# Kernel optimization log

Measured on AMD Instinct MI355X. Metric: run time of the kernel, lower is better.

Reference implementation:

```python
import jax, jax.numpy as jnp
import numpy as np

WS = 7   # window size
SS = 3   # shift size


def _ln(x, g, b):
    m = x.mean(-1, keepdims=True)
    v = ((x - m) ** 2).mean(-1, keepdims=True)
    return (x - m) / jnp.sqrt(v + 1e-5) * g + b


def setup_inputs() -> dict:
    key = jax.random.key(0)
    ks = jax.random.split(key, 8)
    B, H, W, C, nh = 64, 56, 56, 96, 3
    N = WS * WS
    x = jax.random.normal(ks[0], (B, H * W, C), jnp.float32)

    # Swin SW-MSA attention mask: [nW, N, N], 0 where attention is allowed, -100 otherwise
    img = np.zeros((H, W), np.int32)
    cnt = 0
    for hs in (slice(0, H - WS), slice(H - WS, H - SS), slice(H - SS, None)):
        for wsl in (slice(0, W - WS), slice(W - WS, W - SS), slice(W - SS, None)):
            img[hs, wsl] = cnt
            cnt += 1
    win = img.reshape(H // WS, WS, W // WS, WS).transpose(0, 2, 1, 3).reshape(-1, N)
    am = np.where(win[:, None, :] != win[:, :, None], -100.0, 0.0).astype(np.float32)

    # relative position index: [N, N] in [0, (2*WS-1)^2)
    coords = np.stack(np.meshgrid(np.arange(WS), np.arange(WS), indexing='ij')).reshape(2, -1)
    rel = (coords[:, :, None] - coords[:, None, :]).transpose(1, 2, 0)
    rel[..., 0] += WS - 1
    rel[..., 1] += WS - 1
    rel[..., 0] *= 2 * WS - 1
    rel_index = jnp.asarray(rel.sum(-1), jnp.int32)

    p = lambda k, sh: jax.random.normal(k, sh, jnp.float32) * 0.02
    return dict(
        x=x,
        attn_mask=jnp.asarray(am),
        rel_index=rel_index,
        norm1_g=jnp.ones((C,), jnp.float32), norm1_b=jnp.zeros((C,), jnp.float32),
        qkv_w=p(ks[1], (3 * C, C)), qkv_b=jnp.zeros((3 * C,), jnp.float32),
        rel_bias_table=p(ks[2], ((2 * WS - 1) ** 2, nh)),
        proj_w=p(ks[3], (C, C)), proj_b=jnp.zeros((C,), jnp.float32),
        norm2_g=jnp.ones((C,), jnp.float32), norm2_b=jnp.zeros((C,), jnp.float32),
        fc1_w=p(ks[4], (4 * C, C)), fc1_b=jnp.zeros((4 * C,), jnp.float32),
        fc2_w=p(ks[5], (C, 4 * C)), fc2_b=jnp.zeros((C,), jnp.float32),
        H=56, W=56,
    )


def reference(x, attn_mask, rel_index, norm1_g, norm1_b, qkv_w, qkv_b,
              rel_bias_table, proj_w, proj_b, norm2_g, norm2_b,
              fc1_w, fc1_b, fc2_w, fc2_b, H, W):
    B, L, C = x.shape
    nh = rel_bias_table.shape[1]
    d = C // nh
    N = WS * WS
    shortcut = x

    xn = _ln(x, norm1_g, norm1_b).reshape(B, H, W, C)
    # cyclic shift (H%WS==0, W%WS==0 so no padding needed)
    xs = jnp.roll(xn, (-SS, -SS), axis=(1, 2))
    # window partition -> [B*nW, N, C]
    xw = xs.reshape(B, H // WS, WS, W // WS, WS, C).transpose(0, 1, 3, 2, 4, 5).reshape(-1, N, C)
    B_ = xw.shape[0]
    nW = attn_mask.shape[0]

    qkv = (xw @ qkv_w.T + qkv_b).reshape(B_, N, 3, nh, d).transpose(2, 0, 3, 1, 4)
    q, k, v = qkv[0] * (d ** -0.5), qkv[1], qkv[2]  # [B_, nh, N, d]
    attn = jnp.einsum('bhnd,bhmd->bhnm', q, k)
    bias = rel_bias_table[rel_index.reshape(-1)].reshape(N, N, nh).transpose(2, 0, 1)
    attn = attn + bias[None]
    attn = attn.reshape(B_ // nW, nW, nh, N, N) + attn_mask[None, :, None]
    attn = jax.nn.softmax(attn.reshape(B_, nh, N, N), axis=-1)
    out = jnp.einsum('bhnm,bhmd->bhnd', attn, v).transpose(0, 2, 1, 3).reshape(B_, N, C)
    out = out @ proj_w.T + proj_b

    # window reverse + reverse cyclic shift
    xr = out.reshape(B, H // WS, W // WS, WS, WS, C).transpose(0, 1, 3, 2, 4, 5).reshape(B, H, W, C)
    xr = jnp.roll(xr, (SS, SS), axis=(1, 2)).reshape(B, L, C)

    x = shortcut + xr
    h = _ln(x, norm2_g, norm2_b)
    h = jax.nn.gelu(h @ fc1_w.T + fc1_b, approximate=False) @ fc2_w.T + fc2_b
    return x + h
```

## Files before the change

kernel.cpp:

```cpp
#include <hip/hip_runtime.h>
#include <hip/hip_bf16.h>

typedef __attribute__((ext_vector_type(8))) short short8;
typedef __attribute__((ext_vector_type(4))) float f32x4;

constexpr int HW = 56;

constexpr int SR    = 104;
constexpr int SVT   = 200;
constexpr int OFF_X = 0;
constexpr int OFF_Q = 64 * SR;
constexpr int OFF_K = 2 * 64 * SR;
constexpr int OFF_V = 3 * 64 * SR;
constexpr int POOLN = OFF_V + 32 * SVT;

constexpr int WQKV  = 0;
constexpr int WPROJ = 27648;
constexpr int WFC1  = 36864;
constexpr int WFC2  = 73728;
constexpr int WTOT  = 110592;

__device__ __forceinline__ ushort bfc(float f) {
  union { __hip_bfloat16 h; ushort u; } v;
  v.h = __float2bfloat16(f);
  return v.u;
}
__device__ __forceinline__ uint pk2(float a, float b) {
  union { __hip_bfloat162 h2; uint u; } v;
  v.h2 = __float22bfloat162_rn(make_float2(a, b));
  return v.u;
}
__device__ __forceinline__ void st4(short* p, float a, float b, float c, float d) {
  uint2 u; u.x = pk2(a, b); u.y = pk2(c, d);
  *(uint2*)p = u;
}
__device__ __forceinline__ short8 ldw8(const float* p) {
  float4 a = *(const float4*)p;
  float4 b = *(const float4*)(p + 4);
  short8 r;
  r[0] = (short)bfc(a.x); r[1] = (short)bfc(a.y); r[2] = (short)bfc(a.z); r[3] = (short)bfc(a.w);
  r[4] = (short)bfc(b.x); r[5] = (short)bfc(b.y); r[6] = (short)bfc(b.z); r[7] = (short)bfc(b.w);
  return r;
}
template<bool PRE>
__device__ __forceinline__ short8 wfrag(const short* wsb, int ts, int lane, const float* fsrc) {
  if constexpr (PRE) return *(const short8*)&wsb[(ts << 9) + lane * 8];
  else               return ldw8(fsrc);
}
__device__ __forceinline__ float gelu(float v) {
  return v / (1.0f + __expf(-1.702f * v));
}
__device__ __forceinline__ void stage9(const short* g0, short* l0, int wv, int lane) {
  #pragma unroll
  for (int s4 = 0; s4 < 3; ++s4) {
    int s = wv + 4 * s4;
    if (s < 9)
      __builtin_amdgcn_global_load_lds((const unsigned int*)(g0 + (s << 9) + lane * 8),
                                       (unsigned int*)(l0 + (s << 9)), 16, 0, 0);
  }
}

__global__ __launch_bounds__(256) void cvt_weights(
    const float* __restrict__ qkv_w, const float* __restrict__ proj_w,
    const float* __restrict__ fc1_w, const float* __restrict__ fc2_w,
    short* __restrict__ ws)
{
  int idx = blockIdx.x * 256 + threadIdx.x;
  if (idx >= WTOT) return;
  int j = idx & 7, lane = (idx >> 3) & 63;
  int cl = lane & 15;
  int g  = 8 * (lane >> 4) + j;
  float v;
  if (idx < WPROJ) {
    int ts = idx >> 9; int tile = ts / 3, s = ts - 3 * tile;
    v = qkv_w[(size_t)(16 * tile + cl) * 96 + 32 * s + g];
  } else if (idx < WFC1) {
    int ts = (idx - WPROJ) >> 9; int tile = ts / 3, s = ts - 3 * tile;
    v = proj_w[(size_t)(16 * tile + cl) * 96 + 32 * s + g];
  } else if (idx < WFC2) {
    int ts = (idx - WFC1) >> 9; int T = ts / 3, s = ts - 3 * T;
    int cn = T / 6, nt = T - 6 * cn;
    v = fc1_w[(size_t)(96 * cn + 16 * nt + cl) * 96 + 32 * s + g];
  } else {
    int ts = (idx - WFC2) >> 9; int T = ts / 3, s = ts - 3 * T;
    int cn = T / 6, nt = T - 6 * cn;
    v = fc2_w[(size_t)(16 * nt + cl) * 384 + 96 * cn + 32 * s + g];
  }
  ws[idx] = (short)bfc(v);
}

template<bool PRE>
__global__ __launch_bounds__(256, 3) void swin_mfma_kernel(
    const float* __restrict__ x,
    const float* __restrict__ attn_mask,
    const int*   __restrict__ rel_index,
    const float* __restrict__ n1g, const float* __restrict__ n1b,
    const float* __restrict__ qkv_w, const float* __restrict__ qkv_b,
    const float* __restrict__ rel_tab,
    const float* __restrict__ proj_w, const float* __restrict__ proj_b,
    const float* __restrict__ n2g, const float* __restrict__ n2b,
    const float* __restrict__ fc1_w, const float* __restrict__ fc1_b,
    const float* __restrict__ fc2_w, const float* __restrict__ fc2_b,
    const short* __restrict__ wsw,
    float* __restrict__ out)
{
  __shared__ alignas(16) short pool[POOLN];
  short* bufA = (short*)&pool[OFF_K];
  short* bufB = (short*)&pool[OFF_K + 4608];

  const int tid  = threadIdx.x;
  const int wv   = tid >> 6;
  const int lane = tid & 63;
  const int ln   = lane & 15;
  const int gq   = lane >> 4;
  const int bw   = blockIdx.x;
  const int b    = bw >> 6, widx = bw & 63;
  const int wr   = widx >> 3, wc = widx & 7;

  const f32x4 zf = {0.f, 0.f, 0.f, 0.f};
  const int qq = 16 * wv + ln;

  auto gbase = [&](int n) -> size_t {
    int i = n / 7, j = n - 7 * i;
    int h = wr * 7 + i + 3; if (h >= HW) h -= HW;
    int w = wc * 7 + j + 3; if (w >= HW) w -= HW;
    return ((size_t)b * (HW * HW) + (size_t)h * HW + w) * 96;
  };
  const size_t obase = gbase(qq < 49 ? qq : 48);

  float xraw[6][4];
  {
    if (qq < 49) {
      const float* xr = x + obase;
      #pragma unroll
      for (int nt = 0; nt < 6; ++nt) {
        float4 v = *(const float4*)&xr[16 * nt + 4 * gq];
        xraw[nt][0] = v.x; xraw[nt][1] = v.y; xraw[nt][2] = v.z; xraw[nt][3] = v.w;
      }
    } else {
      #pragma unroll
      for (int nt = 0; nt < 6; ++nt)
        xraw[nt][0] = xraw[nt][1] = xraw[nt][2] = xraw[nt][3] = 0.f;
    }
    float s1 = 0.f, s2 = 0.f;
    #pragma unroll
    for (int nt = 0; nt < 6; ++nt)
      #pragma unroll
      for (int r = 0; r < 4; ++r) { s1 += xraw[nt][r]; s2 += xraw[nt][r] * xraw[nt][r]; }
    s1 += __shfl_xor(s1, 16, 64); s1 += __shfl_xor(s1, 32, 64);
    s2 += __shfl_xor(s2, 16, 64); s2 += __shfl_xor(s2, 32, 64);
    float mean = s1 * (1.f / 96.f);
    float inv  = rsqrtf(s2 * (1.f / 96.f) - mean * mean + 1e-5f);
    #pragma unroll
    for (int nt = 0; nt < 6; ++nt) {
      float4 g4 = *(const float4*)&n1g[16 * nt + 4 * gq];
      float4 b4 = *(const float4*)&n1b[16 * nt + 4 * gq];
      st4(&pool[OFF_X + qq * SR + 16 * nt + 4 * gq],
          (xraw[nt][0] - mean) * inv * g4.x + b4.x,
          (xraw[nt][1] - mean) * inv * g4.y + b4.y,
          (xraw[nt][2] - mean) * inv * g4.z + b4.z,
          (xraw[nt][3] - mean) * inv * g4.w + b4.w);
    }
  }
  __syncthreads();

  {
    short8 af[3][4];
    #pragma unroll
    for (int s = 0; s < 3; ++s)
      #pragma unroll
      for (int m = 0; m < 4; ++m)
        af[s][m] = *(const short8*)&pool[OFF_X + (16 * m + ln) * SR + 32 * s + 8 * gq];

    for (int t = wv; t < 18; t += 4) {
      short8 wf[3];
      #pragma unroll
      for (int s = 0; s < 3; ++s)
        wf[s] = wfrag<PRE>(wsw + WQKV, t * 3 + s, lane,
                           qkv_w + (size_t)(16 * t + ln) * 96 + 32 * s + 8 * gq);
      int which = t / 6;
      if (which == 2) {
        int d  = 16 * (t - 12) + ln;
        float bv = qkv_b[192 + d];
        int dd = d & 31, hh = d >> 5;
        #pragma unroll
        for (int m = 0; m < 4; ++m) {
          f32x4 acc = zf;
          #pragma unroll
          for (int s = 0; s < 3; ++s)
            acc = __builtin_amdgcn_mfma_f32_16x16x32_bf16(af[s][m], wf[s], acc, 0, 0, 0);
          st4(&pool[OFF_V + dd * SVT + hh * 64 + 16 * m + 4 * gq],
              acc[0] + bv, acc[1] + bv, acc[2] + bv, acc[3] + bv);
        }
      } else {
        float4 b4 = *(const float4*)&qkv_b[16 * t + 4 * gq];
        #pragma unroll
        for (int m = 0; m < 4; ++m) {
          f32x4 acc = zf;
          #pragma unroll
          for (int s = 0; s < 3; ++s)
            acc = __builtin_amdgcn_mfma_f32_16x16x32_bf16(wf[s], af[s][m], acc, 0, 0, 0);
          int tok = 16 * m + ln;
          float v0 = acc[0] + b4.x, v1 = acc[1] + b4.y, v2 = acc[2] + b4.z, v3 = acc[3] + b4.w;
          if (which == 0) {
            const float sc_ = 0.17677669529663687f;
            st4(&pool[OFF_Q + tok * SR + 16 * t + 4 * gq], v0 * sc_, v1 * sc_, v2 * sc_, v3 * sc_);
          } else {
            st4(&pool[OFF_K + tok * SR + 16 * (t - 6) + 4 * gq], v0, v1, v2, v3);
          }
        }
      }
    }
  }
  __syncthreads();

  int   relvv[4][4];
  float maskb[4][4];
  {
    int qc = qq < 49 ? qq : 48;
    #pragma unroll
    for (int nt = 0; nt < 4; ++nt)
      #pragma unroll
      for (int r = 0; r < 4; ++r) {
        int key = 16 * nt + 4 * gq + r;
        if (key < 49) {
          int qk = qc * 49 + key;
          relvv[nt][r] = rel_index[qk];
          maskb[nt][r] = attn_mask[(size_t)widx * 2401 + qk];
        } else {
          relvv[nt][r] = 0;
          maskb[nt][r] = -1e30f;
        }
      }
  }

  for (int h = 0; h < 3; ++h) {
    short8 bq = *(const short8*)&pool[OFF_Q + qq * SR + h * 32 + 8 * gq];
    f32x4 sc[4];
    #pragma unroll
    for (int nt = 0; nt < 4; ++nt) {
      f32x4 bia;
      #pragma unroll
      for (int r = 0; r < 4; ++r)
        bia[r] = rel_tab[relvv[nt][r] * 3 + h] + maskb[nt][r];
      short8 ak = *(const short8*)&pool[OFF_K + (16 * nt + ln) * SR + h * 32 + 8 * gq];
      sc[nt] = __builtin_amdgcn_mfma_f32_16x16x32_bf16(ak, bq, bia, 0, 0, 0);
    }
    float pv[4][4];
    float sum = 0.f;
    #pragma unroll
    for (int nt = 0; nt < 4; ++nt)
      #pragma unroll
      for (int r = 0; r < 4; ++r) { pv[nt][r] = __expf(sc[nt][r]); sum += pv[nt][r]; }
    sum += __shfl_xor(sum, 16, 64);
    sum += __shfl_xor(sum, 32, 64);
    float inv = 1.f / sum;
    #pragma unroll
    for (int nt = 0; nt < 4; ++nt)
      st4(&pool[OFF_X + qq * SR + 16 * nt + 4 * gq],
          pv[nt][0] * inv, pv[nt][1] * inv, pv[nt][2] * inv, pv[nt][3] * inv);

    short8 bp0 = *(const short8*)&pool[OFF_X + qq * SR + 8 * gq];
    short8 bp1 = *(const short8*)&pool[OFF_X + qq * SR + 32 + 8 * gq];
    #pragma unroll
    for (int dt = 0; dt < 2; ++dt) {
      short8 av0 = *(const short8*)&pool[OFF_V + (16 * dt + ln) * SVT + h * 64 + 8 * gq];
      short8 av1 = *(const short8*)&pool[OFF_V + (16 * dt + ln) * SVT + h * 64 + 32 + 8 * gq];
      f32x4 o = __builtin_amdgcn_mfma_f32_16x16x32_bf16(av0, bp0, zf, 0, 0, 0);
      o = __builtin_amdgcn_mfma_f32_16x16x32_bf16(av1, bp1, o, 0, 0, 0);
      st4(&pool[OFF_Q + qq * SR + h * 32 + 16 * dt + 4 * gq], o[0], o[1], o[2], o[3]);
    }
  }

  short8 ao[3];
  #pragma unroll
  for (int s = 0; s < 3; ++s)
    ao[s] = *(const short8*)&pool[OFF_Q + qq * SR + 32 * s + 8 * gq];
  __syncthreads();

  if constexpr (PRE) stage9(wsw + WPROJ, bufA, wv, lane);
  __syncthreads();

  if constexpr (PRE) stage9(wsw + WPROJ + 9 * 512, bufB, wv, lane);
  float y[6][4];
  #pragma unroll
  for (int nt = 0; nt < 3; ++nt) {
    f32x4 acc = zf;
    #pragma unroll
    for (int s = 0; s < 3; ++s) {
      short8 wfr = PRE ? *(const short8*)&bufA[(nt * 3 + s) * 512 + lane * 8]
                       : ldw8(proj_w + (size_t)(16 * nt + ln) * 96 + 32 * s + 8 * gq);
      acc = __builtin_amdgcn_mfma_f32_16x16x32_bf16(wfr, ao[s], acc, 0, 0, 0);
    }
    float4 pb = *(const float4*)&proj_b[16 * nt + 4 * gq];
    y[nt][0] = acc[0] + pb.x + xraw[nt][0];
    y[nt][1] = acc[1] + pb.y + xraw[nt][1];
    y[nt][2] = acc[2] + pb.z + xraw[nt][2];
    y[nt][3] = acc[3] + pb.w + xraw[nt][3];
  }
  __syncthreads();

  if constexpr (PRE) stage9(wsw + WFC1, bufA, wv, lane);
  #pragma unroll
  for (int nt = 3; nt < 6; ++nt) {
    f32x4 acc = zf;
    #pragma unroll
    for (int s = 0; s < 3; ++s) {
      short8 wfr = PRE ? *(const short8*)&bufB[((nt - 3) * 3 + s) * 512 + lane * 8]
                       : ldw8(proj_w + (size_t)(16 * nt + ln) * 96 + 32 * s + 8 * gq);
      acc = __builtin_amdgcn_mfma_f32_16x16x32_bf16(wfr, ao[s], acc, 0, 0, 0);
    }
    float4 pb = *(const float4*)&proj_b[16 * nt + 4 * gq];
    y[nt][0] = acc[0] + pb.x + xraw[nt][0];
    y[nt][1] = acc[1] + pb.y + xraw[nt][1];
    y[nt][2] = acc[2] + pb.z + xraw[nt][2];
    y[nt][3] = acc[3] + pb.w + xraw[nt][3];
  }
  {
    float s1 = 0.f, s2 = 0.f;
    #pragma unroll
    for (int nt = 0; nt < 6; ++nt)
      #pragma unroll
      for (int r = 0; r < 4; ++r) { s1 += y[nt][r]; s2 += y[nt][r] * y[nt][r]; }
    s1 += __shfl_xor(s1, 16, 64); s1 += __shfl_xor(s1, 32, 64);
    s2 += __shfl_xor(s2, 16, 64); s2 += __shfl_xor(s2, 32, 64);
    float mean = s1 * (1.f / 96.f);
    float inv  = rsqrtf(s2 * (1.f / 96.f) - mean * mean + 1e-5f);
    #pragma unroll
    for (int nt = 0; nt < 6; ++nt) {
      float4 g4 = *(const float4*)&n2g[16 * nt + 4 * gq];
      float4 b4 = *(const float4*)&n2b[16 * nt + 4 * gq];
      st4(&pool[OFF_Q + qq * SR + 16 * nt + 4 * gq],
          (y[nt][0] - mean) * inv * g4.x + b4.x,
          (y[nt][1] - mean) * inv * g4.y + b4.y,
          (y[nt][2] - mean) * inv * g4.z + b4.z,
          (y[nt][3] - mean) * inv * g4.w + b4.w);
    }
  }
  short8 ay[3];
  #pragma unroll
  for (int s = 0; s < 3; ++s)
    ay[s] = *(const short8*)&pool[OFF_Q + qq * SR + 32 * s + 8 * gq];
  __syncthreads();

  f32x4 accO[6] = {zf, zf, zf, zf, zf, zf};
  for (int cn = 0; cn < 4; ++cn) {
    if constexpr (PRE) stage9(wsw + WFC1 + (cn * 18 + 9) * 512, bufB, wv, lane);
    #pragma unroll
    for (int nt = 0; nt < 3; ++nt) {
      f32x4 acc = zf;
      #pragma unroll
      for (int s = 0; s < 3; ++s) {
        short8 wfr = PRE ? *(const short8*)&bufA[(nt * 3 + s) * 512 + lane * 8]
                         : ldw8(fc1_w + (size_t)(96 * cn + 16 * nt + ln) * 96 + 32 * s + 8 * gq);
        acc = __builtin_amdgcn_mfma_f32_16x16x32_bf16(wfr, ay[s], acc, 0, 0, 0);
      }
      float4 b1 = *(const float4*)&fc1_b[96 * cn + 16 * nt + 4 * gq];
      st4(&pool[OFF_X + qq * SR + 16 * nt + 4 * gq],
          gelu(acc[0] + b1.x), gelu(acc[1] + b1.y),
          gelu(acc[2] + b1.z), gelu(acc[3] + b1.w));
    }
    __syncthreads();
    if constexpr (PRE) stage9(wsw + WFC2 + (cn * 18) * 512, bufA, wv, lane);
    #pragma unroll
    for (int nt = 3; nt < 6; ++nt) {
      f32x4 acc = zf;
      #pragma unroll
      for (int s = 0; s < 3; ++s) {
        short8 wfr = PRE ? *(const short8*)&bufB[((nt - 3) * 3 + s) * 512 + lane * 8]
                         : ldw8(fc1_w + (size_t)(96 * cn + 16 * nt + ln) * 96 + 32 * s + 8 * gq);
        acc = __builtin_amdgcn_mfma_f32_16x16x32_bf16(wfr, ay[s], acc, 0, 0, 0);
      }
      float4 b1 = *(const float4*)&fc1_b[96 * cn + 16 * nt + 4 * gq];
      st4(&pool[OFF_X + qq * SR + 16 * nt + 4 * gq],
          gelu(acc[0] + b1.x), gelu(acc[1] + b1.y),
          gelu(acc[2] + b1.z), gelu(acc[3] + b1.w));
    }
    short8 ah[3];
    #pragma unroll
    for (int s = 0; s < 3; ++s)
      ah[s] = *(const short8*)&pool[OFF_X + qq * SR + 32 * s + 8 * gq];
    __syncthreads();
    if constexpr (PRE) stage9(wsw + WFC2 + (cn * 18 + 9) * 512, bufB, wv, lane);
    #pragma unroll
    for (int nt = 0; nt < 3; ++nt) {
      #pragma unroll
      for (int s = 0; s < 3; ++s) {
        short8 wfr = PRE ? *(const short8*)&bufA[(nt * 3 + s) * 512 + lane * 8]
                         : ldw8(fc2_w + (size_t)(16 * nt + ln) * 384 + 96 * cn + 32 * s + 8 * gq);
        accO[nt] = __builtin_amdgcn_mfma_f32_16x16x32_bf16(wfr, ah[s], accO[nt], 0, 0, 0);
      }
    }
    __syncthreads();
    if constexpr (PRE) { if (cn < 3) stage9(wsw + WFC1 + ((cn + 1) * 18) * 512, bufA, wv, lane); }
    #pragma unroll
    for (int nt = 3; nt < 6; ++nt) {
      #pragma unroll
      for (int s = 0; s < 3; ++s) {
        short8 wfr = PRE ? *(const short8*)&bufB[((nt - 3) * 3 + s) * 512 + lane * 8]
                         : ldw8(fc2_w + (size_t)(16 * nt + ln) * 384 + 96 * cn + 32 * s + 8 * gq);
        accO[nt] = __builtin_amdgcn_mfma_f32_16x16x32_bf16(wfr, ah[s], accO[nt], 0, 0, 0);
      }
    }
    __syncthreads();
  }

  if (qq < 49) {
    float* dst = out + obase;
    #pragma unroll
    for (int nt = 0; nt < 6; ++nt) {
      float4 fb = *(const float4*)&fc2_b[16 * nt + 4 * gq];
      float4 v;
      v.x = y[nt][0] + accO[nt][0] + fb.x;
      v.y = y[nt][1] + accO[nt][1] + fb.y;
      v.z = y[nt][2] + accO[nt][2] + fb.z;
      v.w = y[nt][3] + accO[nt][3] + fb.w;
      *(float4*)&dst[16 * nt + 4 * gq] = v;
    }
  }
}

extern "C" void kernel_launch(void* const* d_in, const int* in_sizes, int n_in,
                              void* d_out, int out_size, void* d_ws, size_t ws_size,
                              hipStream_t stream) {
  const float* x         = (const float*)d_in[0];
  const float* attn_mask = (const float*)d_in[1];
  const int*   rel_index = (const int*)  d_in[2];
  const float* n1g       = (const float*)d_in[3];
  const float* n1b       = (const float*)d_in[4];
  const float* qkv_w     = (const float*)d_in[5];
  const float* qkv_b     = (const float*)d_in[6];
  const float* rel_tab   = (const float*)d_in[7];
  const float* proj_w    = (const float*)d_in[8];
  const float* proj_b    = (const float*)d_in[9];
  const float* n2g       = (const float*)d_in[10];
  const float* n2b       = (const float*)d_in[11];
  const float* fc1_w     = (const float*)d_in[12];
  const float* fc1_b     = (const float*)d_in[13];
  const float* fc2_w     = (const float*)d_in[14];
  const float* fc2_b     = (const float*)d_in[15];
  float* out = (float*)d_out;

  const int B = in_sizes[0] / (HW * HW * 96);
  const bool pre = ws_size >= (size_t)WTOT * 2;

  if (pre) {
    short* ws = (short*)d_ws;
    cvt_weights<<<(WTOT + 255) / 256, 256, 0, stream>>>(qkv_w, proj_w, fc1_w, fc2_w, ws);
    swin_mfma_kernel<true><<<B * 64, 256, 0, stream>>>(
        x, attn_mask, rel_index, n1g, n1b, qkv_w, qkv_b, rel_tab, proj_w, proj_b,
        n2g, n2b, fc1_w, fc1_b, fc2_w, fc2_b, (const short*)ws, out);
  } else {
    swin_mfma_kernel<false><<<B * 64, 256, 0, stream>>>(
        x, attn_mask, rel_index, n1g, n1b, qkv_w, qkv_b, rel_tab, proj_w, proj_b,
        n2g, n2b, fc1_w, fc1_b, fc2_w, fc2_b, (const short*)nullptr, out);
  }
}
```

Measured before the change: 170.1 us.

## Precompute combined bias/mask table, fold q scale into weights, add setprio

A new prep kernel builds a per-window, per-head table of relative-position bias plus attention mask, padded to 64 keys. The main kernel then reads one float4 per tile instead of gathering rel_tab through indices and adding the mask. The q scaling is folded into the converted qkv weights and bias. The MFMA regions are wrapped in s_setprio, and the divides in GELU and softmax become rcp intrinsics. This costs an extra kernel launch and about 2.4 MB of workspace, and it depends on the workspace being large enough.

```diff
diff --git a/kernel.cpp b/kernel.cpp
--- a/kernel.cpp
+++ b/kernel.cpp
@@ -19,6 +19,9 @@
 constexpr int WFC1  = 36864;
 constexpr int WFC2  = 73728;
 constexpr int WTOT  = 110592;
+constexpr int BIASN = 64 * 3 * 49 * 64;
+constexpr size_t WS_M1 = (size_t)WTOT * 2;
+constexpr size_t WS_M2 = WS_M1 + (size_t)BIASN * 4;
 
 __device__ __forceinline__ ushort bfc(float f) {
   union { __hip_bfloat16 h; ushort u; } v;
@@ -48,7 +51,7 @@
   else               return ldw8(fsrc);
 }
 __device__ __forceinline__ float gelu(float v) {
-  return v / (1.0f + __expf(-1.702f * v));
+  return v * __builtin_amdgcn_rcpf(1.0f + __expf(-1.702f * v));
 }
 __device__ __forceinline__ void stage9(const short* g0, short* l0, int wv, int lane) {
   #pragma unroll
@@ -74,6 +77,7 @@
   if (idx < WPROJ) {
     int ts = idx >> 9; int tile = ts / 3, s = ts - 3 * tile;
     v = qkv_w[(size_t)(16 * tile + cl) * 96 + 32 * s + g];
+    if (tile < 6) v *= 0.17677669529663687f;
   } else if (idx < WFC1) {
     int ts = (idx - WPROJ) >> 9; int tile = ts / 3, s = ts - 3 * tile;
     v = proj_w[(size_t)(16 * tile + cl) * 96 + 32 * s + g];
@@ -89,7 +93,26 @@
   ws[idx] = (short)bfc(v);
 }
 
-template<bool PRE>
+__global__ __launch_bounds__(256) void prep_bias(
+    const float* __restrict__ attn_mask, const int* __restrict__ rel_index,
+    const float* __restrict__ rel_tab, float* __restrict__ bias3)
+{
+  int idx = blockIdx.x * 256 + threadIdx.x;
+  if (idx >= BIASN) return;
+  int k = idx & 63;
+  int t = idx >> 6;
+  int q = t % 49;
+  int wh = t / 49;
+  int h = wh % 3, w = wh / 3;
+  float v = -1e30f;
+  if (k < 49) {
+    int qk = q * 49 + k;
+    v = rel_tab[rel_index[qk] * 3 + h] + attn_mask[(size_t)w * 2401 + qk];
+  }
+  bias3[idx] = v;
+}
+
+template<int MODE>
 __global__ __launch_bounds__(256, 3) void swin_mfma_kernel(
     const float* __restrict__ x,
     const float* __restrict__ attn_mask,
@@ -102,8 +125,10 @@
     const float* __restrict__ fc1_w, const float* __restrict__ fc1_b,
     const float* __restrict__ fc2_w, const float* __restrict__ fc2_b,
     const short* __restrict__ wsw,
+    const float* __restrict__ bias3,
     float* __restrict__ out)
 {
+  constexpr bool PRE = (MODE >= 1);
   __shared__ alignas(16) short pool[POOLN];
   short* bufA = (short*)&pool[OFF_K];
   short* bufB = (short*)&pool[OFF_K + 4608];
@@ -172,6 +197,7 @@
       for (int m = 0; m < 4; ++m)
         af[s][m] = *(const short8*)&pool[OFF_X + (16 * m + ln) * SR + 32 * s + 8 * gq];
 
+    const float sc_ = 0.17677669529663687f;
     for (int t = wv; t < 18; t += 4) {
       short8 wf[3];
       #pragma unroll
@@ -183,6 +209,7 @@
         int d  = 16 * (t - 12) + ln;
         float bv = qkv_b[192 + d];
         int dd = d & 31, hh = d >> 5;
+        __builtin_amdgcn_s_setprio(1);
         #pragma unroll
         for (int m = 0; m < 4; ++m) {
           f32x4 acc = zf;
@@ -192,8 +219,13 @@
           st4(&pool[OFF_V + dd * SVT + hh * 64 + 16 * m + 4 * gq],
               acc[0] + bv, acc[1] + bv, acc[2] + bv, acc[3] + bv);
         }
+        __builtin_amdgcn_s_setprio(0);
       } else {
         float4 b4 = *(const float4*)&qkv_b[16 * t + 4 * gq];
+        if (which == 0) {
+          if constexpr (PRE) { b4.x *= sc_; b4.y *= sc_; b4.z *= sc_; b4.w *= sc_; }
+        }
+        __builtin_amdgcn_s_setprio(1);
         #pragma unroll
         for (int m = 0; m < 4; ++m) {
           f32x4 acc = zf;
@@ -203,21 +235,24 @@
           int tok = 16 * m + ln;
           float v0 = acc[0] + b4.x, v1 = acc[1] + b4.y, v2 = acc[2] + b4.z, v3 = acc[3] + b4.w;
           if (which == 0) {
-            const float sc_ = 0.17677669529663687f;
-            st4(&pool[OFF_Q + tok * SR + 16 * t + 4 * gq], v0 * sc_, v1 * sc_, v2 * sc_, v3 * sc_);
+            if constexpr (PRE)
+              st4(&pool[OFF_Q + tok * SR + 16 * t + 4 * gq], v0, v1, v2, v3);
+            else
+              st4(&pool[OFF_Q + tok * SR + 16 * t + 4 * gq], v0 * sc_, v1 * sc_, v2 * sc_, v3 * sc_);
           } else {
             st4(&pool[OFF_K + tok * SR + 16 * (t - 6) + 4 * gq], v0, v1, v2, v3);
           }
         }
+        __builtin_amdgcn_s_setprio(0);
       }
     }
   }
   __syncthreads();
 
+  const int qc = qq < 49 ? qq : 48;
   int   relvv[4][4];
   float maskb[4][4];
-  {
-    int qc = qq < 49 ? qq : 48;
+  if constexpr (MODE < 2) {
     #pragma unroll
     for (int nt = 0; nt < 4; ++nt)
       #pragma unroll
@@ -233,19 +268,27 @@
         }
       }
   }
+  const float* bph = nullptr;
+  if constexpr (MODE == 2) bph = bias3 + ((size_t)widx * 3 * 49 + qc) * 64;
 
   for (int h = 0; h < 3; ++h) {
     short8 bq = *(const short8*)&pool[OFF_Q + qq * SR + h * 32 + 8 * gq];
     f32x4 sc[4];
+    __builtin_amdgcn_s_setprio(1);
     #pragma unroll
     for (int nt = 0; nt < 4; ++nt) {
       f32x4 bia;
-      #pragma unroll
-      for (int r = 0; r < 4; ++r)
-        bia[r] = rel_tab[relvv[nt][r] * 3 + h] + maskb[nt][r];
+      if constexpr (MODE == 2) {
+        bia = *(const f32x4*)&bph[h * 3136 + 16 * nt + 4 * gq];
+      } else {
+        #pragma unroll
+        for (int r = 0; r < 4; ++r)
+          bia[r] = rel_tab[relvv[nt][r] * 3 + h] + maskb[nt][r];
+      }
       short8 ak = *(const short8*)&pool[OFF_K + (16 * nt + ln) * SR + h * 32 + 8 * gq];
       sc[nt] = __builtin_amdgcn_mfma_f32_16x16x32_bf16(ak, bq, bia, 0, 0, 0);
     }
+    __builtin_amdgcn_s_setprio(0);
     float pv[4][4];
     float sum = 0.f;
     #pragma unroll
@@ -254,7 +297,7 @@
       for (int r = 0; r < 4; ++r) { pv[nt][r] = __expf(sc[nt][r]); sum += pv[nt][r]; }
     sum += __shfl_xor(sum, 16, 64);
     sum += __shfl_xor(sum, 32, 64);
-    float inv = 1.f / sum;
+    float inv = __builtin_amdgcn_rcpf(sum);
     #pragma unroll
     for (int nt = 0; nt < 4; ++nt)
       st4(&pool[OFF_X + qq * SR + 16 * nt + 4 * gq],
@@ -262,6 +305,7 @@
 
     short8 bp0 = *(const short8*)&pool[OFF_X + qq * SR + 8 * gq];
     short8 bp1 = *(const short8*)&pool[OFF_X + qq * SR + 32 + 8 * gq];
+    __builtin_amdgcn_s_setprio(1);
     #pragma unroll
     for (int dt = 0; dt < 2; ++dt) {
       short8 av0 = *(const short8*)&pool[OFF_V + (16 * dt + ln) * SVT + h * 64 + 8 * gq];
@@ -270,6 +314,7 @@
       o = __builtin_amdgcn_mfma_f32_16x16x32_bf16(av1, bp1, o, 0, 0, 0);
       st4(&pool[OFF_Q + qq * SR + h * 32 + 16 * dt + 4 * gq], o[0], o[1], o[2], o[3]);
     }
+    __builtin_amdgcn_s_setprio(0);
   }
 
   short8 ao[3];
@@ -283,6 +328,7 @@
 
   if constexpr (PRE) stage9(wsw + WPROJ + 9 * 512, bufB, wv, lane);
   float y[6][4];
+  __builtin_amdgcn_s_setprio(1);
   #pragma unroll
   for (int nt = 0; nt < 3; ++nt) {
     f32x4 acc = zf;
@@ -298,9 +344,11 @@
     y[nt][2] = acc[2] + pb.z + xraw[nt][2];
     y[nt][3] = acc[3] + pb.w + xraw[nt][3];
   }
+  __builtin_amdgcn_s_setprio(0);
   __syncthreads();
 
   if constexpr (PRE) stage9(wsw + WFC1, bufA, wv, lane);
+  __builtin_amdgcn_s_setprio(1);
   #pragma unroll
   for (int nt = 3; nt < 6; ++nt) {
     f32x4 acc = zf;
@@ -316,6 +364,7 @@
     y[nt][2] = acc[2] + pb.z + xraw[nt][2];
     y[nt][3] = acc[3] + pb.w + xraw[nt][3];
   }
+  __builtin_amdgcn_s_setprio(0);
   {
     float s1 = 0.f, s2 = 0.f;
     #pragma unroll
@@ -346,6 +395,7 @@
   f32x4 accO[6] = {zf, zf, zf, zf, zf, zf};
   for (int cn = 0; cn < 4; ++cn) {
     if constexpr (PRE) stage9(wsw + WFC1 + (cn * 18 + 9) * 512, bufB, wv, lane);
+    __builtin_amdgcn_s_setprio(1);
     #pragma unroll
     for (int nt = 0; nt < 3; ++nt) {
       f32x4 acc = zf;
@@ -360,8 +410,10 @@
           gelu(acc[0] + b1.x), gelu(acc[1] + b1.y),
           gelu(acc[2] + b1.z), gelu(acc[3] + b1.w));
     }
+    __builtin_amdgcn_s_setprio(0);
     __syncthreads();
     if constexpr (PRE) stage9(wsw + WFC2 + (cn * 18) * 512, bufA, wv, lane);
+    __builtin_amdgcn_s_setprio(1);
     #pragma unroll
     for (int nt = 3; nt < 6; ++nt) {
       f32x4 acc = zf;
@@ -376,12 +428,14 @@
           gelu(acc[0] + b1.x), gelu(acc[1] + b1.y),
           gelu(acc[2] + b1.z), gelu(acc[3] + b1.w));
     }
+    __builtin_amdgcn_s_setprio(0);
     short8 ah[3];
     #pragma unroll
     for (int s = 0; s < 3; ++s)
       ah[s] = *(const short8*)&pool[OFF_X + qq * SR + 32 * s + 8 * gq];
     __syncthreads();
     if constexpr (PRE) stage9(wsw + WFC2 + (cn * 18 + 9) * 512, bufB, wv, lane);
+    __builtin_amdgcn_s_setprio(1);
     #pragma unroll
     for (int nt = 0; nt < 3; ++nt) {
       #pragma unroll
@@ -391,8 +445,10 @@
         accO[nt] = __builtin_amdgcn_mfma_f32_16x16x32_bf16(wfr, ah[s], accO[nt], 0, 0, 0);
       }
     }
+    __builtin_amdgcn_s_setprio(0);
     __syncthreads();
     if constexpr (PRE) { if (cn < 3) stage9(wsw + WFC1 + ((cn + 1) * 18) * 512, bufA, wv, lane); }
+    __builtin_amdgcn_s_setprio(1);
     #pragma unroll
     for (int nt = 3; nt < 6; ++nt) {
       #pragma unroll
@@ -402,6 +458,7 @@
         accO[nt] = __builtin_amdgcn_mfma_f32_16x16x32_bf16(wfr, ah[s], accO[nt], 0, 0, 0);
       }
     }
+    __builtin_amdgcn_s_setprio(0);
     __syncthreads();
   }
 
@@ -442,17 +499,26 @@
   float* out = (float*)d_out;
 
   const int B = in_sizes[0] / (HW * HW * 96);
-  const bool pre = ws_size >= (size_t)WTOT * 2;
-
-  if (pre) {
-    short* ws = (short*)d_ws;
+  const bool m1 = ws_size >= WS_M1;
+  const bool m2 = ws_size >= WS_M2;
+  short* ws    = (short*)d_ws;
+  float* bias3 = (float*)((char*)d_ws + WS_M1);
+
+  if (m1)
     cvt_weights<<<(WTOT + 255) / 256, 256, 0, stream>>>(qkv_w, proj_w, fc1_w, fc2_w, ws);
-    swin_mfma_kernel<true><<<B * 64, 256, 0, stream>>>(
+  if (m2)
+    prep_bias<<<(BIASN + 255) / 256, 256, 0, stream>>>(attn_mask, rel_index, rel_tab, bias3);
+
+  if (m2)
+    swin_mfma_kernel<2><<<B * 64, 256, 0, stream>>>(
         x, attn_mask, rel_index, n1g, n1b, qkv_w, qkv_b, rel_tab, proj_w, proj_b,
-        n2g, n2b, fc1_w, fc1_b, fc2_w, fc2_b, (const short*)ws, out);
-  } else {
-    swin_mfma_kernel<false><<<B * 64, 256, 0, stream>>>(
+        n2g, n2b, fc1_w, fc1_b, fc2_w, fc2_b, (const short*)ws, (const float*)bias3, out);
+  else if (m1)
+    swin_mfma_kernel<1><<<B * 64, 256, 0, stream>>>(
         x, attn_mask, rel_index, n1g, n1b, qkv_w, qkv_b, rel_tab, proj_w, proj_b,
-        n2g, n2b, fc1_w, fc1_b, fc2_w, fc2_b, (const short*)nullptr, out);
-  }
-}
+        n2g, n2b, fc1_w, fc1_b, fc2_w, fc2_b, (const short*)ws, (const float*)nullptr, out);
+  else
+    swin_mfma_kernel<0><<<B * 64, 256, 0, stream>>>(
+        x, attn_mask, rel_index, n1g, n1b, qkv_w, qkv_b, rel_tab, proj_w, proj_b,
+        n2g, n2b, fc1_w, fc1_b, fc2_w, fc2_b, (const short*)nullptr, (const float*)nullptr, out);
+}
```

New measurement: 155.9 us. -8.3%, faster.
